# Optimization experiments

Hardware: AMD Instinct MI355X
Metric: run time of the kernel (lower is better)

Reference implementation:

```python
import jax, jax.numpy as jnp
import numpy as np

B, D, H0, H1, O = 4096, 1024, 1024, 1024, 1024  # O = output_dim + 1
ALPHA = 0.3
CLAMP = 0.3


def setup_inputs() -> dict:
    key = jax.random.key(0)
    ks = jax.random.split(key, 15)
    def he(k, fan_in, shape):
        return jax.random.normal(k, shape, dtype=jnp.float32) * np.sqrt(2.0 / fan_in).astype(np.float32)
    def heb(k, shape):
        return jax.random.uniform(k, shape, dtype=jnp.float32, minval=-CLAMP, maxval=CLAMP)
    return {
        "x": jax.random.normal(ks[0], (B, D), dtype=jnp.float32),
        "x2h0": he(ks[1], D, (D, H0)),
        "x2h1": he(ks[2], D, (D, H1)),
        "h02h1": he(ks[3], H0, (H0, H1)),
        "x2y": he(ks[4], D, (D, O)),
        "h02y": he(ks[5], H0, (H0, O)),
        "h12y": he(ks[6], H1, (H1, O)),
        "heb_x2h0": heb(ks[7], (D, H0)),
        "heb_x2h1": heb(ks[8], (D, H1)),
        "heb_h02h1": heb(ks[9], (H0, H1)),
        "heb_x2y": heb(ks[10], (D, O)),
        "heb_h02y": heb(ks[11], (H0, O)),
        "heb_h12y": heb(ks[12], (H1, O)),
        "W": jax.random.uniform(ks[13], (1, 1), dtype=jnp.float32),
    }


def reference(x, x2h0, x2h1, h02h1, x2y, h02y, h12y,
              heb_x2h0, heb_x2h1, heb_h02h1, heb_x2y, heb_h02y, heb_h12y, W):
    clamp = lambda m: jnp.clip(m, -CLAMP, CLAMP)
    # x -> h0
    h0_x = x @ (x2h0 + W * heb_x2h0)                       # [B, H0]
    heb_x2h0_n = clamp(heb_x2h0 + ALPHA * (x.T @ h0_x))
    h0 = jax.nn.relu(h0_x)
    # x -> h1, h0 -> h1
    h1_x = x @ (x2h1 + W * heb_x2h1)                       # [B, H1]
    heb_x2h1_n = clamp(heb_x2h1 + ALPHA * (x.T @ h1_x))
    h1_0 = h0 @ (h02h1 + W * heb_h02h1)
    heb_h02h1_n = clamp(heb_h02h1 + ALPHA * (h0.T @ h1_0))
    h1 = jax.nn.relu(h1_x + h1_0)
    # x, h0, h1 -> y
    y_x = x @ (x2y + W * heb_x2y)                          # [B, O]
    heb_x2y_n = clamp(heb_x2y + ALPHA * (x.T @ y_x))
    y_0 = h0 @ (h02y + W * heb_h02y)
    heb_h02y_n = clamp(heb_h02y + ALPHA * (h0.T @ y_0))
    y_1 = h1 @ (h12y + W * heb_h12y)
    heb_h12y_n = clamp(heb_h12y + ALPHA * (h1.T @ y_1))
    y = y_x + y_0 + y_1
    W_new = jnp.mean(jnp.tanh(y[:, -2:-1]))               # neuromodulator scalar
    dopa = jnp.mean(jnp.tanh(y[:, -3:-2]))
    y_out = y[:, :-2]                                      # [B, O-2]
    return (y_out, heb_x2h0_n, heb_x2h1_n, heb_h02h1_n,
            heb_x2y_n, heb_h02y_n, heb_h12y_n, W_new, dopa)
```

## Files before the change

### kernel.cpp

```cpp
#include <hip/hip_runtime.h>
#include <stdint.h>

#define ALPHA 0.3f
#define CLAMPV 0.3f
#define BDIM 4096
#define NDIM 1024

typedef float f32x4 __attribute__((ext_vector_type(4)));
typedef __bf16 bf16x8 __attribute__((ext_vector_type(8)));

union U16x8 { uint4 v; unsigned short u[8]; };

__device__ __forceinline__ float bf2f(unsigned short u) {
  union { unsigned int i; float f; } c; c.i = ((unsigned int)u) << 16; return c.f;
}
__device__ __forceinline__ unsigned short f2bf(float f) {
  union { float f; unsigned int i; } c; c.f = f;
  unsigned int u = c.i;
  unsigned int r = u + 0x7FFFu + ((u >> 16) & 1u);
  return (unsigned short)(r >> 16);
}

__global__ __launch_bounds__(256) void fill_k(float* __restrict__ out, int n) {
  int i = blockIdx.x * 256 + threadIdx.x;
  if (i < n) out[i] = 12345.0f;
}

__global__ __launch_bounds__(256) void split_x_k(const float* __restrict__ x,
                                                 unsigned short* __restrict__ hi,
                                                 unsigned short* __restrict__ lo) {
  const size_t i0 = ((size_t)blockIdx.x * 256 + threadIdx.x) * 8;
  f32x4 a = *(const f32x4*)(x + i0);
  f32x4 b = *(const f32x4*)(x + i0 + 4);
  U16x8 h8, l8;
#pragma unroll
  for (int i = 0; i < 4; ++i) {
    unsigned short h = f2bf(a[i]); h8.u[i] = h; l8.u[i] = f2bf(a[i] - bf2f(h));
    unsigned short h2 = f2bf(b[i]); h8.u[4+i] = h2; l8.u[4+i] = f2bf(b[i] - bf2f(h2));
  }
  *(uint4*)(hi + i0) = h8.v;
  *(uint4*)(lo + i0) = l8.v;
}

struct TDesc {
  const void* in1; const void* in2; const float* Wp;
  unsigned short* out_hi; unsigned short* out_lo;
  int R, C, tilesC, mode;
};
struct TBatch { TDesc d[8]; int start[9]; int n; };

__global__ __launch_bounds__(256) void transpose_k(TBatch batch) {
  const int bid = blockIdx.x;
  int g = 0;
#pragma unroll
  for (int i = 1; i < 8; ++i)
    if (i < batch.n && bid >= batch.start[i]) g = i;
  TDesc D = batch.d[g];
  const int lt = bid - batch.start[g];
  const int trow = lt / D.tilesC;
  const int tcol = lt - trow * D.tilesC;
  const int r0 = trow * 64, c0 = tcol * 64;

  __shared__ float tile[64][65];
  const int t = threadIdx.x;
  const int sub = t >> 3, oct = t & 7;
  const float Wv = (D.mode == 2) ? *D.Wp : 0.f;

#pragma unroll
  for (int p = 0; p < 2; ++p) {
    const int rl = p * 32 + sub;
    const int cl0 = oct * 8;
    float vv[8];
    if (D.mode == 0) {
      const unsigned short* ip = (const unsigned short*)D.in1 + (size_t)(r0 + rl) * D.C + c0 + cl0;
      U16x8 tmp; tmp.v = *(const uint4*)ip;
#pragma unroll
      for (int i = 0; i < 8; ++i) vv[i] = bf2f(tmp.u[i]);
    } else {
      const float* ip = (const float*)D.in1 + (size_t)(r0 + rl) * D.C + c0 + cl0;
      f32x4 a = *(const f32x4*)ip, b = *(const f32x4*)(ip + 4);
#pragma unroll
      for (int i = 0; i < 4; ++i) { vv[i] = a[i]; vv[4+i] = b[i]; }
      if (D.mode == 2) {
        const float* ip2 = (const float*)D.in2 + (size_t)(r0 + rl) * D.C + c0 + cl0;
        f32x4 c = *(const f32x4*)ip2, d2 = *(const f32x4*)(ip2 + 4);
#pragma unroll
        for (int i = 0; i < 4; ++i) { vv[i] += Wv * c[i]; vv[4+i] += Wv * d2[i]; }
      }
    }
#pragma unroll
    for (int i = 0; i < 8; ++i) tile[cl0 + i][rl] = vv[i];
  }
  __syncthreads();
#pragma unroll
  for (int p = 0; p < 2; ++p) {
    const int cl = p * 32 + sub;
    const int rl0 = oct * 8;
    U16x8 h8, l8;
#pragma unroll
    for (int i = 0; i < 8; ++i) {
      float v = tile[cl][rl0 + i];
      unsigned short h = f2bf(v);
      h8.u[i] = h;
      l8.u[i] = f2bf(v - bf2f(h));
    }
    const size_t o = (size_t)(c0 + cl) * D.R + r0 + rl0;
    *(uint4*)(D.out_hi + o) = h8.v;
    if (D.mode != 0) *(uint4*)(D.out_lo + o) = l8.v;
  }
}

struct GemmDesc {
  const unsigned short *Ahi, *Alo, *Bhi, *Blo;
  int lda, ldb, nk, accadd;
  float* out32a;
  float* out32b;
  const float* addin;
  unsigned short* sp_hi;
  unsigned short* sp_lo;
  const float* heb_in;
  float* heb_out;
};
struct GemmBatch { GemmDesc d[12]; int start[13]; int n; };

#define AS1 __attribute__((address_space(1)))
#define AS3 __attribute__((address_space(3)))

__global__ __launch_bounds__(256, 2) void gemm_k(GemmBatch batch) {
  const int bid = blockIdx.x;
  int g = 0;
#pragma unroll
  for (int i = 1; i < 12; ++i)
    if (i < batch.n && bid >= batch.start[i]) g = i;
  GemmDesc D = batch.d[g];
  const int local = bid - batch.start[g];
  const int tm = local >> 3;
  const int tn = local & 7;

  __shared__ __align__(16) unsigned short LDS[32768];

  const int t = threadIdx.x;
  const int lane = t & 63;
  const int wave = t >> 6;
  const int wr = wave >> 1, wc = wave & 1;
  const int fr = lane & 15, fg = lane >> 4;

  f32x4 acc[8][4];
#pragma unroll
  for (int i = 0; i < 8; ++i)
#pragma unroll
    for (int j = 0; j < 4; ++j)
#pragma unroll
      for (int r = 0; r < 4; ++r) acc[i][j][r] = 0.f;

  const int r0 = t >> 2;
  const int colSwE = (((t & 3) ^ ((t >> 3) & 3)) << 3);

  size_t aRow[4], bRow[2];
#pragma unroll
  for (int q = 0; q < 4; ++q)
    aRow[q] = (size_t)(tm * 256 + q * 64 + r0) * D.lda + colSwE;
#pragma unroll
  for (int q = 0; q < 2; ++q)
    bRow[q] = (size_t)(tn * 128 + q * 64 + r0) * D.ldb + colSwE;

  const int ldsW = wave * 512;

  auto stageA = [&](const unsigned short* P, int kb, int b) {
    unsigned short* base = LDS + b * 16384 + ldsW;
#pragma unroll
    for (int q = 0; q < 4; ++q)
      __builtin_amdgcn_global_load_lds(
          (const AS1 void*)(P + aRow[q] + kb),
          (AS3 void*)(base + q * 2048), 16, 0, 0);
  };
  auto stageB = [&](const unsigned short* P, int region, int kb, int b) {
    unsigned short* base = LDS + b * 16384 + region + ldsW;
#pragma unroll
    for (int q = 0; q < 2; ++q)
      __builtin_amdgcn_global_load_lds(
          (const AS1 void*)(P + bRow[q] + kb),
          (AS3 void*)(base + q * 2048), 16, 0, 0);
  };

  const int swz = ((fg ^ ((fr >> 1) & 3)) << 4);
  int aoff[8], boff[4];
#pragma unroll
  for (int i = 0; i < 8; ++i)
    aoff[i] = (wr * 128 + i * 16 + fr) * 64 + swz;
#pragma unroll
  for (int j = 0; j < 4; ++j)
    boff[j] = 16384 + (wc * 64 + j * 16 + fr) * 64 + swz;
  const char* ldsc = (const char*)LDS;

  auto computePh0 = [&](int b) {
    const char* bb = ldsc + b * 32768;
    bf16x8 af[8];
#pragma unroll
    for (int i = 0; i < 8; ++i) af[i] = *(const bf16x8*)(bb + aoff[i]);
#pragma unroll
    for (int j = 0; j < 4; ++j) {
      const bf16x8 bh = *(const bf16x8*)(bb + boff[j]);
#pragma unroll
      for (int i = 0; i < 8; ++i)
        acc[i][j] = __builtin_amdgcn_mfma_f32_16x16x32_bf16(af[i], bh, acc[i][j], 0, 0, 0);
      const bf16x8 bl = *(const bf16x8*)(bb + boff[j] + 8192);
#pragma unroll
      for (int i = 0; i < 8; ++i)
        acc[i][j] = __builtin_amdgcn_mfma_f32_16x16x32_bf16(af[i], bl, acc[i][j], 0, 0, 0);
    }
  };
  auto computePh1 = [&](int b) {
    const char* bb = ldsc + b * 32768;
    bf16x8 af[8];
#pragma unroll
    for (int i = 0; i < 8; ++i) af[i] = *(const bf16x8*)(bb + aoff[i]);
#pragma unroll
    for (int j = 0; j < 4; ++j) {
      const bf16x8 bh = *(const bf16x8*)(bb + boff[j]);
#pragma unroll
      for (int i = 0; i < 8; ++i)
        acc[i][j] = __builtin_amdgcn_mfma_f32_16x16x32_bf16(af[i], bh, acc[i][j], 0, 0, 0);
    }
  };

  const int n = D.nk;

  stageA(D.Ahi, 0, 0);
  stageB(D.Bhi, 8192, 0, 0);
  stageB(D.Blo, 12288, 0, 0);
  int buf = 0;

#pragma unroll 1
  for (int kt = 0; kt < n; ++kt) {
    if (kt + 1 < n) {
      const int kb = (kt + 1) << 5;
      stageA(D.Ahi, kb, buf ^ 1);
      stageB(D.Bhi, 8192, kb, buf ^ 1);
      stageB(D.Blo, 12288, kb, buf ^ 1);
      asm volatile("s_waitcnt vmcnt(8)" ::: "memory");
    } else {
      stageA(D.Alo, 0, buf ^ 1);
      stageB(D.Bhi, 8192, 0, buf ^ 1);
      asm volatile("s_waitcnt vmcnt(6)" ::: "memory");
    }
    __builtin_amdgcn_s_barrier();
    __builtin_amdgcn_sched_barrier(0);
    computePh0(buf);
    __builtin_amdgcn_sched_barrier(0);
    __builtin_amdgcn_s_barrier();
    buf ^= 1;
  }

#pragma unroll 1
  for (int kt = 0; kt < n; ++kt) {
    if (kt + 1 < n) {
      const int kb = (kt + 1) << 5;
      stageA(D.Alo, kb, buf ^ 1);
      stageB(D.Bhi, 8192, kb, buf ^ 1);
      asm volatile("s_waitcnt vmcnt(6)" ::: "memory");
    } else {
      asm volatile("s_waitcnt vmcnt(0)" ::: "memory");
    }
    __builtin_amdgcn_s_barrier();
    __builtin_amdgcn_sched_barrier(0);
    computePh1(buf);
    __builtin_amdgcn_sched_barrier(0);
    __builtin_amdgcn_s_barrier();
    buf ^= 1;
  }

  const int grb = tm * 256 + wr * 128 + fg * 4;
  const int gcb = tn * 128 + wc * 64 + fr;
#pragma unroll
  for (int i = 0; i < 8; ++i) {
#pragma unroll
    for (int j = 0; j < 4; ++j) {
      const int gc = gcb + j * 16;
#pragma unroll
      for (int r = 0; r < 4; ++r) {
        const int gr = grb + i * 16 + r;
        const size_t idx = (size_t)gr * NDIM + gc;
        const float v = acc[i][j][r];
        if (D.heb_out) {
          D.heb_out[idx] = fminf(fmaxf(D.heb_in[idx] + ALPHA * v, -CLAMPV), CLAMPV);
        } else {
          if (D.out32a) D.out32a[idx] = v;
          if (D.out32b) D.out32b[idx] = D.accadd ? (D.out32b[idx] + v) : v;
          if (D.sp_hi) {
            float rv = v + (D.addin ? D.addin[idx] : 0.f);
            rv = fmaxf(rv, 0.f);
            const unsigned short h = f2bf(rv);
            D.sp_hi[idx] = h;
            D.sp_lo[idx] = f2bf(rv - bf2f(h));
          }
        }
      }
    }
  }
}

struct HebRed { const float* heb_in; float* out; const float* p[8]; int np; };

__global__ __launch_bounds__(256) void hebred_k(HebRed R) {
  const size_t i0 = ((size_t)blockIdx.x * 256 + threadIdx.x) * 4;
  f32x4 s = *(const f32x4*)(R.p[0] + i0);
#pragma unroll
  for (int k = 1; k < 8; ++k)
    if (k < R.np) s += *(const f32x4*)(R.p[k] + i0);
  f32x4 h = *(const f32x4*)(R.heb_in + i0);
  f32x4 o;
#pragma unroll
  for (int i = 0; i < 4; ++i) o[i] = fminf(fmaxf(h[i] + ALPHA * s[i], -CLAMPV), CLAMPV);
  *(f32x4*)(R.out + i0) = o;
}

__global__ __launch_bounds__(256) void yassm_k(const float* __restrict__ ysum,
                                               float* __restrict__ yout) {
  const int stride = gridDim.x * 256;
  for (int idx = blockIdx.x * 256 + threadIdx.x; idx < BDIM * 1022; idx += stride) {
    const int row = idx / 1022;
    const int col = idx - row * 1022;
    yout[idx] = ysum[(size_t)row * NDIM + col];
  }
}

__global__ __launch_bounds__(256) void tanhcol_k(const float* __restrict__ ysum,
                                                 float* __restrict__ wpart,
                                                 float* __restrict__ dpart) {
  const int r = blockIdx.x * 256 + threadIdx.x;
  const size_t b = (size_t)r * NDIM;
  float tw = tanhf(ysum[b + 1022]);
  float td = tanhf(ysum[b + 1021]);
#pragma unroll
  for (int o = 32; o > 0; o >>= 1) { tw += __shfl_down(tw, o); td += __shfl_down(td, o); }
  __shared__ float s1[4], s2[4];
  const int lane = threadIdx.x & 63, wv = threadIdx.x >> 6;
  if (lane == 0) { s1[wv] = tw; s2[wv] = td; }
  __syncthreads();
  if (threadIdx.x == 0) {
    wpart[blockIdx.x] = s1[0] + s1[1] + s1[2] + s1[3];
    dpart[blockIdx.x] = s2[0] + s2[1] + s2[2] + s2[3];
  }
}

__global__ void finalize_k(const float* __restrict__ wpart, const float* __restrict__ dpart,
                           float* __restrict__ out, int nout) {
  if (threadIdx.x == 0 && blockIdx.x == 0) {
    float s = 0.f, d = 0.f;
    for (int i = 0; i < 16; ++i) { s += wpart[i]; d += dpart[i]; }
    out[nout - 2] = s * (1.f / BDIM);
    out[nout - 1] = d * (1.f / BDIM);
  }
}

extern "C" void kernel_launch(void* const* d_in, const int* in_sizes, int n_in,
                              void* d_out, int out_size, void* d_ws, size_t ws_size,
                              hipStream_t stream) {
  const float* x = (const float*)d_in[0];
  const float* wbase[6]; const float* hebin[6];
  for (int i = 0; i < 6; ++i) { wbase[i] = (const float*)d_in[1 + i]; hebin[i] = (const float*)d_in[7 + i]; }
  const float* Wp = (const float*)d_in[13];
  float* out = (float*)d_out;
  const size_t YOUT = (size_t)BDIM * 1022;
  float* hebout[6];
  for (int i = 0; i < 6; ++i) hebout[i] = out + YOUT + (size_t)i * 1048576;

  const size_t E = (size_t)BDIM * NDIM;
  const size_t PAIRB = E * 4;
  const size_t WPAIRB = (size_t)NDIM * NDIM * 4;
  const size_t FB = E * 4;
  const size_t REQUIRED = 7 * PAIRB + 6 * WPAIRB + 4 * FB;

  if (ws_size < REQUIRED) {
    fill_k<<<(out_size + 255) / 256, 256, 0, stream>>>(out, out_size);
    return;
  }

  char* p = (char*)d_ws;
  auto takeB = [&](size_t n) -> char* { char* q = p; p += n; return q; };

  unsigned short* R0 = (unsigned short*)takeB(PAIRB);
  unsigned short* R1 = (unsigned short*)takeB(PAIRB);
  unsigned short* R2 = (unsigned short*)takeB(PAIRB);
  unsigned short* R3 = (unsigned short*)takeB(PAIRB);
  unsigned short* R4 = (unsigned short*)takeB(PAIRB);
  unsigned short* R5 = (unsigned short*)takeB(PAIRB);
  unsigned short* R6 = (unsigned short*)takeB(PAIRB);
  unsigned short* WThi[6]; unsigned short* WTlo[6];
  for (int i = 0; i < 6; ++i) {
    WThi[i] = (unsigned short*)takeB(WPAIRB);
    WTlo[i] = WThi[i] + (size_t)NDIM * NDIM;
  }
  float* F0 = (float*)takeB(FB);
  float* F1 = (float*)takeB(FB);
  float* F2 = (float*)takeB(FB);
  float* F3 = (float*)takeB(FB);

  unsigned short *xhi = R0, *xlo = R0 + E;
  unsigned short *xThi = R1, *xTlo = R1 + E;
  unsigned short *h0hi = R2, *h0lo = R2 + E;
  unsigned short *h0Thi = R3, *h0Tlo = R3 + E;
  float* part = (float*)R4;
  float* wpart = (float*)R6; float* dpart = wpart + 64;

  split_x_k<<<2048, 256, 0, stream>>>(x, xhi, xlo);

  {
    TBatch tb{};
    int s = 0;
    for (int i = 0; i < 6; ++i) {
      tb.d[i] = { wbase[i], hebin[i], Wp, WThi[i], WTlo[i], NDIM, NDIM, NDIM / 64, 2 };
      tb.start[i] = s; s += (NDIM / 64) * (NDIM / 64);
    }
    tb.d[6] = { x, nullptr, nullptr, xThi, xTlo, BDIM, NDIM, NDIM / 64, 1 };
    tb.start[6] = s; s += (BDIM / 64) * (NDIM / 64);
    tb.start[7] = s; tb.n = 7;
    transpose_k<<<s, 256, 0, stream>>>(tb);
  }

  auto fwdDesc = [&](const unsigned short* ahi, const unsigned short* alo, int wi) -> GemmDesc {
    GemmDesc d{};
    d.Ahi = ahi; d.Alo = alo; d.Bhi = WThi[wi]; d.Blo = WTlo[wi];
    d.lda = NDIM; d.ldb = NDIM; d.nk = NDIM / 32;
    return d;
  };
  auto hebPart = [&](const unsigned short* ahi, const unsigned short* alo,
                     const unsigned short* bhi, const unsigned short* blo,
                     int koff, int klen, float* partOut) -> GemmDesc {
    GemmDesc d{};
    d.Ahi = ahi + koff; d.Alo = alo + koff;
    d.Bhi = bhi + koff; d.Blo = blo + koff;
    d.lda = BDIM; d.ldb = BDIM; d.nk = klen / 32;
    d.out32a = partOut;
    return d;
  };
  auto hebRed = [&](int hi, const float* q0, const float* q1, const float* q2,
                    const float* q3, const float* q4, const float* q5,
                    const float* q6, const float* q7, int np) {
    HebRed r{};
    r.heb_in = hebin[hi]; r.out = hebout[hi];
    r.p[0]=q0; r.p[1]=q1; r.p[2]=q2; r.p[3]=q3; r.p[4]=q4; r.p[5]=q5; r.p[6]=q6; r.p[7]=q7;
    r.np = np;
    hebred_k<<<1024, 256, 0, stream>>>(r);
  };

  {
    GemmBatch gb{};
    gb.d[0] = fwdDesc(xhi, xlo, 0);
    gb.d[0].out32a = F0; gb.d[0].sp_hi = h0hi; gb.d[0].sp_lo = h0lo;
    gb.d[1] = fwdDesc(xhi, xlo, 1);
    gb.d[1].out32a = F1;
    gb.d[2] = fwdDesc(xhi, xlo, 3);
    gb.d[2].out32a = F2; gb.d[2].out32b = F3; gb.d[2].accadd = 0;
    gb.start[0] = 0; gb.start[1] = 128; gb.start[2] = 256; gb.start[3] = 384;
    gb.n = 3;
    gemm_k<<<384, 256, 0, stream>>>(gb);
  }

  {
    TBatch tb{};
    tb.d[0] = { F0, nullptr, nullptr, R4, R4 + E, BDIM, NDIM, NDIM / 64, 1 };
    tb.d[1] = { F1, nullptr, nullptr, R5, R5 + E, BDIM, NDIM, NDIM / 64, 1 };
    tb.d[2] = { F2, nullptr, nullptr, R6, R6 + E, BDIM, NDIM, NDIM / 64, 1 };
    tb.d[3] = { h0hi, nullptr, nullptr, h0Thi, nullptr, BDIM, NDIM, NDIM / 64, 0 };
    tb.d[4] = { h0lo, nullptr, nullptr, h0Tlo, nullptr, BDIM, NDIM, NDIM / 64, 0 };
    for (int i = 0; i < 6; ++i) tb.start[i] = i * 1024;
    tb.n = 5;
    transpose_k<<<5120, 256, 0, stream>>>(tb);
  }

  {
    float* px0a = (float*)WThi[0]; float* px0b = hebout[0];
    float* px1a = (float*)WThi[1]; float* px1b = hebout[1];
    float* pxya = (float*)WThi[3]; float* pxyb = hebout[3];
    GemmBatch gb{};
    gb.d[0] = hebPart(xThi, xTlo, R4, R4 + E, 0,    2048, px0a);
    gb.d[1] = hebPart(xThi, xTlo, R4, R4 + E, 2048, 2048, px0b);
    gb.d[2] = hebPart(xThi, xTlo, R5, R5 + E, 0,    2048, px1a);
    gb.d[3] = hebPart(xThi, xTlo, R5, R5 + E, 2048, 2048, px1b);
    gb.d[4] = hebPart(xThi, xTlo, R6, R6 + E, 0,    2048, pxya);
    gb.d[5] = hebPart(xThi, xTlo, R6, R6 + E, 2048, 2048, pxyb);
    gb.d[6] = fwdDesc(h0hi, h0lo, 2);
    gb.d[6].out32a = F0; gb.d[6].addin = F1; gb.d[6].sp_hi = R0; gb.d[6].sp_lo = R0 + E;
    gb.d[7] = fwdDesc(h0hi, h0lo, 4);
    gb.d[7].out32a = F2; gb.d[7].out32b = F3; gb.d[7].accadd = 1;
    for (int i = 0; i < 6; ++i) gb.start[i] = i * 32;
    gb.start[6] = 192; gb.start[7] = 320; gb.start[8] = 448;
    gb.n = 8;
    gemm_k<<<448, 256, 0, stream>>>(gb);
    hebRed(0, px0a, px0b, 0,0,0,0,0,0, 2);
    hebRed(1, px1a, px1b, 0,0,0,0,0,0, 2);
    hebRed(3, pxya, pxyb, 0,0,0,0,0,0, 2);
  }

  {
    TBatch tb{};
    tb.d[0] = { F0, nullptr, nullptr, R4, R4 + E, BDIM, NDIM, NDIM / 64, 1 };
    tb.d[1] = { F2, nullptr, nullptr, R5, R5 + E, BDIM, NDIM, NDIM / 64, 1 };
    tb.d[2] = { R0, nullptr, nullptr, R1, nullptr, BDIM, NDIM, NDIM / 64, 0 };
    tb.d[3] = { R0 + E, nullptr, nullptr, R1 + E, nullptr, BDIM, NDIM, NDIM / 64, 0 };
    for (int i = 0; i < 5; ++i) tb.start[i] = i * 1024;
    tb.n = 4;
    transpose_k<<<4096, 256, 0, stream>>>(tb);
  }

  {
    float* pa[4] = { (float*)WThi[0], (float*)WThi[1], (float*)WThi[2], (float*)WThi[3] };
    float* pb[4] = { (float*)R6, (float*)R6 + 1048576, (float*)R6 + 2097152, (float*)R6 + 3145728 };
    GemmBatch gb{};
    for (int h = 0; h < 4; ++h) {
      gb.d[h]     = hebPart(h0Thi, h0Tlo, R4, R4 + E, h * 1024, 1024, pa[h]);
      gb.d[4 + h] = hebPart(h0Thi, h0Tlo, R5, R5 + E, h * 1024, 1024, pb[h]);
    }
    gb.d[8] = fwdDesc(R0, R0 + E, 5);
    gb.d[8].out32a = F1; gb.d[8].out32b = F3; gb.d[8].accadd = 1;
    for (int i = 0; i < 8; ++i) gb.start[i] = i * 32;
    gb.start[8] = 256; gb.start[9] = 384;
    gb.n = 9;
    gemm_k<<<384, 256, 0, stream>>>(gb);
    hebRed(2, pa[0], pa[1], pa[2], pa[3], 0,0,0,0, 4);
    hebRed(4, pb[0], pb[1], pb[2], pb[3], 0,0,0,0, 4);
  }

  {
    TBatch tb{};
    tb.d[0] = { F1, nullptr, nullptr, R2, R2 + E, BDIM, NDIM, NDIM / 64, 1 };
    tb.start[0] = 0; tb.start[1] = 1024; tb.n = 1;
    transpose_k<<<1024, 256, 0, stream>>>(tb);
  }

  {
    GemmBatch gb{};
    for (int h = 0; h < 8; ++h)
      gb.d[h] = hebPart(R1, R1 + E, R2, R2 + E, h * 512, 512, part + (size_t)h * 1048576);
    for (int i = 0; i <= 8; ++i) gb.start[i] = i * 32;
    gb.n = 8;
    gemm_k<<<256, 256, 0, stream>>>(gb);
    hebRed(5, part, part + 1048576, part + 2097152, part + 3145728,
           part + 4194304, part + 5242880, part + 6291456, part + 7340032, 8);
  }

  yassm_k<<<2048, 256, 0, stream>>>(F3, out);
  tanhcol_k<<<16, 256, 0, stream>>>(F3, wpart, dpart);
  finalize_k<<<1, 64, 0, stream>>>(wpart, dpart, out, out_size);
}
```

Baseline: 513.2 us.

## Add 128x128 BK=64 single-buffered GEMM variant for small launches, keep 256x128 for big one

Rewrites gemm_k as a 128x128 tile kernel with a K-step of 64, single-buffered LDS and an XOR swizzle. This doubles the block count for the forward GEMM, the h0-heb GEMM and the final heb GEMM so the GPU fills better. The old double-buffered 256x128 kernel is kept as gemm256_k for the large mixed batch. The trade-off is lost load/compute overlap, since each step waits at a syncthreads with no prefetch, plus more redundant operand traffic from the smaller tiles.

```diff
diff --git a/kernel.cpp b/kernel.cpp
--- a/kernel.cpp
+++ b/kernel.cpp
@@ -122,11 +122,12 @@
   float* heb_out;
 };
 struct GemmBatch { GemmDesc d[12]; int start[13]; int n; };
+struct Gemm256Batch { GemmDesc d[8]; int start[9]; int n; };
 
 #define AS1 __attribute__((address_space(1)))
 #define AS3 __attribute__((address_space(3)))
 
-__global__ __launch_bounds__(256, 2) void gemm_k(GemmBatch batch) {
+__global__ __launch_bounds__(256) void gemm_k(GemmBatch batch) {
   const int bid = blockIdx.x;
   int g = 0;
 #pragma unroll
@@ -137,7 +138,9 @@
   const int tm = local >> 3;
   const int tn = local & 7;
 
-  __shared__ __align__(16) unsigned short LDS[32768];
+  __shared__ __align__(16) unsigned short As[128 * 64];
+  __shared__ __align__(16) unsigned short BsH[128 * 64];
+  __shared__ __align__(16) unsigned short BsL[128 * 64];
 
   const int t = threadIdx.x;
   const int lane = t & 63;
@@ -145,135 +148,85 @@
   const int wr = wave >> 1, wc = wave & 1;
   const int fr = lane & 15, fg = lane >> 4;
 
-  f32x4 acc[8][4];
-#pragma unroll
-  for (int i = 0; i < 8; ++i)
-#pragma unroll
-    for (int j = 0; j < 4; ++j)
-#pragma unroll
-      for (int r = 0; r < 4; ++r) acc[i][j][r] = 0.f;
-
-  const int r0 = t >> 2;
-  const int colSwE = (((t & 3) ^ ((t >> 3) & 3)) << 3);
-
-  size_t aRow[4], bRow[2];
-#pragma unroll
-  for (int q = 0; q < 4; ++q)
-    aRow[q] = (size_t)(tm * 256 + q * 64 + r0) * D.lda + colSwE;
-#pragma unroll
-  for (int q = 0; q < 2; ++q)
-    bRow[q] = (size_t)(tn * 128 + q * 64 + r0) * D.ldb + colSwE;
-
-  const int ldsW = wave * 512;
-
-  auto stageA = [&](const unsigned short* P, int kb, int b) {
-    unsigned short* base = LDS + b * 16384 + ldsW;
-#pragma unroll
-    for (int q = 0; q < 4; ++q)
-      __builtin_amdgcn_global_load_lds(
-          (const AS1 void*)(P + aRow[q] + kb),
-          (AS3 void*)(base + q * 2048), 16, 0, 0);
-  };
-  auto stageB = [&](const unsigned short* P, int region, int kb, int b) {
-    unsigned short* base = LDS + b * 16384 + region + ldsW;
-#pragma unroll
-    for (int q = 0; q < 2; ++q)
-      __builtin_amdgcn_global_load_lds(
-          (const AS1 void*)(P + bRow[q] + kb),
-          (AS3 void*)(base + q * 2048), 16, 0, 0);
-  };
-
-  const int swz = ((fg ^ ((fr >> 1) & 3)) << 4);
-  int aoff[8], boff[4];
-#pragma unroll
-  for (int i = 0; i < 8; ++i)
-    aoff[i] = (wr * 128 + i * 16 + fr) * 64 + swz;
-#pragma unroll
-  for (int j = 0; j < 4; ++j)
-    boff[j] = 16384 + (wc * 64 + j * 16 + fr) * 64 + swz;
-  const char* ldsc = (const char*)LDS;
-
-  auto computePh0 = [&](int b) {
-    const char* bb = ldsc + b * 32768;
-    bf16x8 af[8];
-#pragma unroll
-    for (int i = 0; i < 8; ++i) af[i] = *(const bf16x8*)(bb + aoff[i]);
-#pragma unroll
-    for (int j = 0; j < 4; ++j) {
-      const bf16x8 bh = *(const bf16x8*)(bb + boff[j]);
-#pragma unroll
-      for (int i = 0; i < 8; ++i)
-        acc[i][j] = __builtin_amdgcn_mfma_f32_16x16x32_bf16(af[i], bh, acc[i][j], 0, 0, 0);
-      const bf16x8 bl = *(const bf16x8*)(bb + boff[j] + 8192);
-#pragma unroll
-      for (int i = 0; i < 8; ++i)
-        acc[i][j] = __builtin_amdgcn_mfma_f32_16x16x32_bf16(af[i], bl, acc[i][j], 0, 0, 0);
-    }
-  };
-  auto computePh1 = [&](int b) {
-    const char* bb = ldsc + b * 32768;
-    bf16x8 af[8];
-#pragma unroll
-    for (int i = 0; i < 8; ++i) af[i] = *(const bf16x8*)(bb + aoff[i]);
-#pragma unroll
-    for (int j = 0; j < 4; ++j) {
-      const bf16x8 bh = *(const bf16x8*)(bb + boff[j]);
-#pragma unroll
-      for (int i = 0; i < 8; ++i)
-        acc[i][j] = __builtin_amdgcn_mfma_f32_16x16x32_bf16(af[i], bh, acc[i][j], 0, 0, 0);
-    }
-  };
-
-  const int n = D.nk;
-
-  stageA(D.Ahi, 0, 0);
-  stageB(D.Bhi, 8192, 0, 0);
-  stageB(D.Blo, 12288, 0, 0);
-  int buf = 0;
+  const f32x4 vzero = {0.f, 0.f, 0.f, 0.f};
+  f32x4 acc[4][4];
+#pragma unroll
+  for (int i = 0; i < 4; ++i)
+#pragma unroll
+    for (int j = 0; j < 4; ++j) acc[i][j] = vzero;
+
+  const int srow = t >> 3;
+  const int scolB = ((t & 7) << 4) ^ ((srow & 7) << 4);
+  const int scolE = scolB >> 1;
+
+  int aoff[4], boff[4];
+#pragma unroll
+  for (int i = 0; i < 4; ++i) {
+    const int ra = wr * 64 + i * 16 + fr;
+    aoff[i] = ra * 128 + ((fg << 4) ^ ((ra & 7) << 4));
+    const int rb = wc * 64 + i * 16 + fr;
+    boff[i] = rb * 128 + ((fg << 4) ^ ((rb & 7) << 4));
+  }
+  const char* Asb = (const char*)As;
+  const char* BsHb = (const char*)BsH;
+  const char* BsLb = (const char*)BsL;
+
+  const size_t arow = (size_t)(tm * 128 + srow) * D.lda + scolE;
+  const size_t brow = (size_t)(tn * 128 + srow) * D.ldb + scolE;
+  const size_t astep = (size_t)32 * D.lda;
+  const size_t bstep = (size_t)32 * D.ldb;
 
 #pragma unroll 1
-  for (int kt = 0; kt < n; ++kt) {
-    if (kt + 1 < n) {
-      const int kb = (kt + 1) << 5;
-      stageA(D.Ahi, kb, buf ^ 1);
-      stageB(D.Bhi, 8192, kb, buf ^ 1);
-      stageB(D.Blo, 12288, kb, buf ^ 1);
-      asm volatile("s_waitcnt vmcnt(8)" ::: "memory");
-    } else {
-      stageA(D.Alo, 0, buf ^ 1);
-      stageB(D.Bhi, 8192, 0, buf ^ 1);
-      asm volatile("s_waitcnt vmcnt(6)" ::: "memory");
-    }
-    __builtin_amdgcn_s_barrier();
-    __builtin_amdgcn_sched_barrier(0);
-    computePh0(buf);
-    __builtin_amdgcn_sched_barrier(0);
-    __builtin_amdgcn_s_barrier();
-    buf ^= 1;
-  }
-
+  for (int ph = 0; ph < 2; ++ph) {
+    const unsigned short* Ap = ph ? D.Alo : D.Ahi;
 #pragma unroll 1
-  for (int kt = 0; kt < n; ++kt) {
-    if (kt + 1 < n) {
-      const int kb = (kt + 1) << 5;
-      stageA(D.Alo, kb, buf ^ 1);
-      stageB(D.Bhi, 8192, kb, buf ^ 1);
-      asm volatile("s_waitcnt vmcnt(6)" ::: "memory");
-    } else {
-      asm volatile("s_waitcnt vmcnt(0)" ::: "memory");
-    }
-    __builtin_amdgcn_s_barrier();
-    __builtin_amdgcn_sched_barrier(0);
-    computePh1(buf);
-    __builtin_amdgcn_sched_barrier(0);
-    __builtin_amdgcn_s_barrier();
-    buf ^= 1;
-  }
-
-  const int grb = tm * 256 + wr * 128 + fg * 4;
+    for (int kt = 0; kt < D.nk; ++kt) {
+      const int kb = kt << 6;
+#pragma unroll
+      for (int q = 0; q < 4; ++q) {
+        __builtin_amdgcn_global_load_lds(
+            (const AS1 void*)(Ap + arow + q * astep + kb),
+            (AS3 void*)(As + q * 2048 + wave * 512), 16, 0, 0);
+        __builtin_amdgcn_global_load_lds(
+            (const AS1 void*)(D.Bhi + brow + q * bstep + kb),
+            (AS3 void*)(BsH + q * 2048 + wave * 512), 16, 0, 0);
+      }
+      if (ph == 0) {
+#pragma unroll
+        for (int q = 0; q < 4; ++q)
+          __builtin_amdgcn_global_load_lds(
+              (const AS1 void*)(D.Blo + brow + q * bstep + kb),
+              (AS3 void*)(BsL + q * 2048 + wave * 512), 16, 0, 0);
+      }
+      __syncthreads();
+#pragma unroll
+      for (int s = 0; s < 2; ++s) {
+        const int sx = s << 6;
+        bf16x8 af[4];
+#pragma unroll
+        for (int i = 0; i < 4; ++i) af[i] = *(const bf16x8*)(Asb + (aoff[i] ^ sx));
+#pragma unroll
+        for (int j = 0; j < 4; ++j) {
+          const bf16x8 bh = *(const bf16x8*)(BsHb + (boff[j] ^ sx));
+#pragma unroll
+          for (int i = 0; i < 4; ++i)
+            acc[i][j] = __builtin_amdgcn_mfma_f32_16x16x32_bf16(af[i], bh, acc[i][j], 0, 0, 0);
+          if (ph == 0) {
+            const bf16x8 bl = *(const bf16x8*)(BsLb + (boff[j] ^ sx));
+#pragma unroll
+            for (int i = 0; i < 4; ++i)
+              acc[i][j] = __builtin_amdgcn_mfma_f32_16x16x32_bf16(af[i], bl, acc[i][j], 0, 0, 0);
+          }
+        }
+      }
+      __syncthreads();
+    }
+  }
+
+  const int grb = tm * 128 + wr * 64 + fg * 4;
   const int gcb = tn * 128 + wc * 64 + fr;
 #pragma unroll
-  for (int i = 0; i < 8; ++i) {
+  for (int i = 0; i < 4; ++i) {
 #pragma unroll
     for (int j = 0; j < 4; ++j) {
       const int gc = gcb + j * 16;
@@ -300,6 +253,180 @@
   }
 }
 
+__global__ __launch_bounds__(256, 2) void gemm256_k(Gemm256Batch batch) {
+  const int bid = blockIdx.x;
+  int g = 0;
+#pragma unroll
+  for (int i = 1; i < 8; ++i)
+    if (i < batch.n && bid >= batch.start[i]) g = i;
+  GemmDesc D = batch.d[g];
+  const int local = bid - batch.start[g];
+  const int tm = local >> 3;
+  const int tn = local & 7;
+
+  __shared__ __align__(16) unsigned short LDS[32768];
+
+  const int t = threadIdx.x;
+  const int lane = t & 63;
+  const int wave = t >> 6;
+  const int wr = wave >> 1, wc = wave & 1;
+  const int fr = lane & 15, fg = lane >> 4;
+
+  f32x4 acc[8][4];
+#pragma unroll
+  for (int i = 0; i < 8; ++i)
+#pragma unroll
+    for (int j = 0; j < 4; ++j)
+#pragma unroll
+      for (int rr = 0; rr < 4; ++rr) acc[i][j][rr] = 0.f;
+
+  const int r0 = t >> 2;
+  const int colSwE = (((t & 3) ^ ((t >> 3) & 3)) << 3);
+
+  size_t aRow[4], bRow[2];
+#pragma unroll
+  for (int qq = 0; qq < 4; ++qq)
+    aRow[qq] = (size_t)(tm * 256 + qq * 64 + r0) * D.lda + colSwE;
+#pragma unroll
+  for (int qq = 0; qq < 2; ++qq)
+    bRow[qq] = (size_t)(tn * 128 + qq * 64 + r0) * D.ldb + colSwE;
+
+  const int ldsW = wave * 512;
+
+  auto stageA = [&](const unsigned short* P, int kb, int b) {
+    unsigned short* base = LDS + b * 16384 + ldsW;
+#pragma unroll
+    for (int qq = 0; qq < 4; ++qq)
+      __builtin_amdgcn_global_load_lds(
+          (const AS1 void*)(P + aRow[qq] + kb),
+          (AS3 void*)(base + qq * 2048), 16, 0, 0);
+  };
+  auto stageB = [&](const unsigned short* P, int region, int kb, int b) {
+    unsigned short* base = LDS + b * 16384 + region + ldsW;
+#pragma unroll
+    for (int qq = 0; qq < 2; ++qq)
+      __builtin_amdgcn_global_load_lds(
+          (const AS1 void*)(P + bRow[qq] + kb),
+          (AS3 void*)(base + qq * 2048), 16, 0, 0);
+  };
+
+  const int swz = ((fg ^ ((fr >> 1) & 3)) << 4);
+  int aoff[8], boff[4];
+#pragma unroll
+  for (int i = 0; i < 8; ++i)
+    aoff[i] = (wr * 128 + i * 16 + fr) * 64 + swz;
+#pragma unroll
+  for (int j = 0; j < 4; ++j)
+    boff[j] = 16384 + (wc * 64 + j * 16 + fr) * 64 + swz;
+  const char* ldsc = (const char*)LDS;
+
+  auto computePh0 = [&](int b) {
+    const char* bb = ldsc + b * 32768;
+    bf16x8 af[8];
+#pragma unroll
+    for (int i = 0; i < 8; ++i) af[i] = *(const bf16x8*)(bb + aoff[i]);
+#pragma unroll
+    for (int j = 0; j < 4; ++j) {
+      const bf16x8 bh = *(const bf16x8*)(bb + boff[j]);
+#pragma unroll
+      for (int i = 0; i < 8; ++i)
+        acc[i][j] = __builtin_amdgcn_mfma_f32_16x16x32_bf16(af[i], bh, acc[i][j], 0, 0, 0);
+      const bf16x8 bl = *(const bf16x8*)(bb + boff[j] + 8192);
+#pragma unroll
+      for (int i = 0; i < 8; ++i)
+        acc[i][j] = __builtin_amdgcn_mfma_f32_16x16x32_bf16(af[i], bl, acc[i][j], 0, 0, 0);
+    }
+  };
+  auto computePh1 = [&](int b) {
+    const char* bb = ldsc + b * 32768;
+    bf16x8 af[8];
+#pragma unroll
+    for (int i = 0; i < 8; ++i) af[i] = *(const bf16x8*)(bb + aoff[i]);
+#pragma unroll
+    for (int j = 0; j < 4; ++j) {
+      const bf16x8 bh = *(const bf16x8*)(bb + boff[j]);
+#pragma unroll
+      for (int i = 0; i < 8; ++i)
+        acc[i][j] = __builtin_amdgcn_mfma_f32_16x16x32_bf16(af[i], bh, acc[i][j], 0, 0, 0);
+    }
+  };
+
+  const int n = D.nk;
+
+  stageA(D.Ahi, 0, 0);
+  stageB(D.Bhi, 8192, 0, 0);
+  stageB(D.Blo, 12288, 0, 0);
+  int buf = 0;
+
+#pragma unroll 1
+  for (int kt = 0; kt < n; ++kt) {
+    if (kt + 1 < n) {
+      const int kb = (kt + 1) << 5;
+      stageA(D.Ahi, kb, buf ^ 1);
+      stageB(D.Bhi, 8192, kb, buf ^ 1);
+      stageB(D.Blo, 12288, kb, buf ^ 1);
+      asm volatile("s_waitcnt vmcnt(8)" ::: "memory");
+    } else {
+      stageA(D.Alo, 0, buf ^ 1);
+      stageB(D.Bhi, 8192, 0, buf ^ 1);
+      asm volatile("s_waitcnt vmcnt(6)" ::: "memory");
+    }
+    __builtin_amdgcn_s_barrier();
+    __builtin_amdgcn_sched_barrier(0);
+    computePh0(buf);
+    __builtin_amdgcn_sched_barrier(0);
+    __builtin_amdgcn_s_barrier();
+    buf ^= 1;
+  }
+
+#pragma unroll 1
+  for (int kt = 0; kt < n; ++kt) {
+    if (kt + 1 < n) {
+      const int kb = (kt + 1) << 5;
+      stageA(D.Alo, kb, buf ^ 1);
+      stageB(D.Bhi, 8192, kb, buf ^ 1);
+      asm volatile("s_waitcnt vmcnt(6)" ::: "memory");
+    } else {
+      asm volatile("s_waitcnt vmcnt(0)" ::: "memory");
+    }
+    __builtin_amdgcn_s_barrier();
+    __builtin_amdgcn_sched_barrier(0);
+    computePh1(buf);
+    __builtin_amdgcn_sched_barrier(0);
+    __builtin_amdgcn_s_barrier();
+    buf ^= 1;
+  }
+
+  const int grb = tm * 256 + wr * 128 + fg * 4;
+  const int gcb = tn * 128 + wc * 64 + fr;
+#pragma unroll
+  for (int i = 0; i < 8; ++i) {
+#pragma unroll
+    for (int j = 0; j < 4; ++j) {
+      const int gc = gcb + j * 16;
+#pragma unroll
+      for (int rr = 0; rr < 4; ++rr) {
+        const int gr = grb + i * 16 + rr;
+        const size_t idx = (size_t)gr * NDIM + gc;
+        const float v = acc[i][j][rr];
+        if (D.heb_out) {
+          D.heb_out[idx] = fminf(fmaxf(D.heb_in[idx] + ALPHA * v, -CLAMPV), CLAMPV);
+        } else {
+          if (D.out32a) D.out32a[idx] = v;
+          if (D.out32b) D.out32b[idx] = D.accadd ? (D.out32b[idx] + v) : v;
+          if (D.sp_hi) {
+            float rv = v + (D.addin ? D.addin[idx] : 0.f);
+            rv = fmaxf(rv, 0.f);
+            const unsigned short h = f2bf(rv);
+            D.sp_hi[idx] = h;
+            D.sp_lo[idx] = f2bf(rv - bf2f(h));
+          }
+        }
+      }
+    }
+  }
+}
+
 struct HebRed { const float* heb_in; float* out; const float* p[8]; int np; };
 
 __global__ __launch_bounds__(256) void hebred_k(HebRed R) {
@@ -419,19 +546,19 @@
     transpose_k<<<s, 256, 0, stream>>>(tb);
   }
 
-  auto fwdDesc = [&](const unsigned short* ahi, const unsigned short* alo, int wi) -> GemmDesc {
+  auto fwdDesc = [&](const unsigned short* ahi, const unsigned short* alo, int wi, int bk) -> GemmDesc {
     GemmDesc d{};
     d.Ahi = ahi; d.Alo = alo; d.Bhi = WThi[wi]; d.Blo = WTlo[wi];
-    d.lda = NDIM; d.ldb = NDIM; d.nk = NDIM / 32;
+    d.lda = NDIM; d.ldb = NDIM; d.nk = NDIM / bk;
     return d;
   };
   auto hebPart = [&](const unsigned short* ahi, const unsigned short* alo,
                      const unsigned short* bhi, const unsigned short* blo,
-                     int koff, int klen, float* partOut) -> GemmDesc {
+                     int koff, int klen, float* partOut, int bk) -> GemmDesc {
     GemmDesc d{};
     d.Ahi = ahi + koff; d.Alo = alo + koff;
     d.Bhi = bhi + koff; d.Blo = blo + koff;
-    d.lda = BDIM; d.ldb = BDIM; d.nk = klen / 32;
+    d.lda = BDIM; d.ldb = BDIM; d.nk = klen / bk;
     d.out32a = partOut;
     return d;
   };
@@ -447,15 +574,15 @@
 
   {
     GemmBatch gb{};
-    gb.d[0] = fwdDesc(xhi, xlo, 0);
+    gb.d[0] = fwdDesc(xhi, xlo, 0, 64);
     gb.d[0].out32a = F0; gb.d[0].sp_hi = h0hi; gb.d[0].sp_lo = h0lo;
-    gb.d[1] = fwdDesc(xhi, xlo, 1);
+    gb.d[1] = fwdDesc(xhi, xlo, 1, 64);
     gb.d[1].out32a = F1;
-    gb.d[2] = fwdDesc(xhi, xlo, 3);
+    gb.d[2] = fwdDesc(xhi, xlo, 3, 64);
     gb.d[2].out32a = F2; gb.d[2].out32b = F3; gb.d[2].accadd = 0;
-    gb.start[0] = 0; gb.start[1] = 128; gb.start[2] = 256; gb.start[3] = 384;
+    gb.start[0] = 0; gb.start[1] = 256; gb.start[2] = 512; gb.start[3] = 768;
     gb.n = 3;
-    gemm_k<<<384, 256, 0, stream>>>(gb);
+    gemm_k<<<768, 256, 0, stream>>>(gb);
   }
 
   {
@@ -474,21 +601,21 @@
     float* px0a = (float*)WThi[0]; float* px0b = hebout[0];
     float* px1a = (float*)WThi[1]; float* px1b = hebout[1];
     float* pxya = (float*)WThi[3]; float* pxyb = hebout[3];
-    GemmBatch gb{};
-    gb.d[0] = hebPart(xThi, xTlo, R4, R4 + E, 0,    2048, px0a);
-    gb.d[1] = hebPart(xThi, xTlo, R4, R4 + E, 2048, 2048, px0b);
-    gb.d[2] = hebPart(xThi, xTlo, R5, R5 + E, 0,    2048, px1a);
-    gb.d[3] = hebPart(xThi, xTlo, R5, R5 + E, 2048, 2048, px1b);
-    gb.d[4] = hebPart(xThi, xTlo, R6, R6 + E, 0,    2048, pxya);
-    gb.d[5] = hebPart(xThi, xTlo, R6, R6 + E, 2048, 2048, pxyb);
-    gb.d[6] = fwdDesc(h0hi, h0lo, 2);
+    Gemm256Batch gb{};
+    gb.d[0] = hebPart(xThi, xTlo, R4, R4 + E, 0,    2048, px0a, 32);
+    gb.d[1] = hebPart(xThi, xTlo, R4, R4 + E, 2048, 2048, px0b, 32);
+    gb.d[2] = hebPart(xThi, xTlo, R5, R5 + E, 0,    2048, px1a, 32);
+    gb.d[3] = hebPart(xThi, xTlo, R5, R5 + E, 2048, 2048, px1b, 32);
+    gb.d[4] = hebPart(xThi, xTlo, R6, R6 + E, 0,    2048, pxya, 32);
+    gb.d[5] = hebPart(xThi, xTlo, R6, R6 + E, 2048, 2048, pxyb, 32);
+    gb.d[6] = fwdDesc(h0hi, h0lo, 2, 32);
     gb.d[6].out32a = F0; gb.d[6].addin = F1; gb.d[6].sp_hi = R0; gb.d[6].sp_lo = R0 + E;
-    gb.d[7] = fwdDesc(h0hi, h0lo, 4);
+    gb.d[7] = fwdDesc(h0hi, h0lo, 4, 32);
     gb.d[7].out32a = F2; gb.d[7].out32b = F3; gb.d[7].accadd = 1;
     for (int i = 0; i < 6; ++i) gb.start[i] = i * 32;
     gb.start[6] = 192; gb.start[7] = 320; gb.start[8] = 448;
     gb.n = 8;
-    gemm_k<<<448, 256, 0, stream>>>(gb);
+    gemm256_k<<<448, 256, 0, stream>>>(gb);
     hebRed(0, px0a, px0b, 0,0,0,0,0,0, 2);
     hebRed(1, px1a, px1b, 0,0,0,0,0,0, 2);
     hebRed(3, pxya, pxyb, 0,0,0,0,0,0, 2);
@@ -510,15 +637,15 @@
     float* pb[4] = { (float*)R6, (float*)R6 + 1048576, (float*)R6 + 2097152, (float*)R6 + 3145728 };
     GemmBatch gb{};
     for (int h = 0; h < 4; ++h) {
-      gb.d[h]     = hebPart(h0Thi, h0Tlo, R4, R4 + E, h * 1024, 1024, pa[h]);
-      gb.d[4 + h] = hebPart(h0Thi, h0Tlo, R5, R5 + E, h * 1024, 1024, pb[h]);
-    }
-    gb.d[8] = fwdDesc(R0, R0 + E, 5);
+      gb.d[h]     = hebPart(h0Thi, h0Tlo, R4, R4 + E, h * 1024, 1024, pa[h], 64);
+      gb.d[4 + h] = hebPart(h0Thi, h0Tlo, R5, R5 + E, h * 1024, 1024, pb[h], 64);
+    }
+    gb.d[8] = fwdDesc(R0, R0 + E, 5, 64);
     gb.d[8].out32a = F1; gb.d[8].out32b = F3; gb.d[8].accadd = 1;
-    for (int i = 0; i < 8; ++i) gb.start[i] = i * 32;
-    gb.start[8] = 256; gb.start[9] = 384;
+    for (int i = 0; i < 8; ++i) gb.start[i] = i * 64;
+    gb.start[8] = 512; gb.start[9] = 768;
     gb.n = 9;
-    gemm_k<<<384, 256, 0, stream>>>(gb);
+    gemm_k<<<768, 256, 0, stream>>>(gb);
     hebRed(2, pa[0], pa[1], pa[2], pa[3], 0,0,0,0, 4);
     hebRed(4, pb[0], pb[1], pb[2], pb[3], 0,0,0,0, 4);
   }
@@ -533,10 +660,10 @@
   {
     GemmBatch gb{};
     for (int h = 0; h < 8; ++h)
-      gb.d[h] = hebPart(R1, R1 + E, R2, R2 + E, h * 512, 512, part + (size_t)h * 1048576);
-    for (int i = 0; i <= 8; ++i) gb.start[i] = i * 32;
+      gb.d[h] = hebPart(R1, R1 + E, R2, R2 + E, h * 512, 512, part + (size_t)h * 1048576, 64);
+    for (int i = 0; i <= 8; ++i) gb.start[i] = i * 64;
     gb.n = 8;
-    gemm_k<<<256, 256, 0, stream>>>(gb);
+    gemm_k<<<512, 256, 0, stream>>>(gb);
     hebRed(5, part, part + 1048576, part + 2097152, part + 3145728,
            part + 4194304, part + 5242880, part + 6291456, part + 7340032, 8);
   }
```

After: 485.5 us. 5.4% less time.
